# Kernel optimization log

Hardware: AMD Instinct MI355X
Metric: run time of the kernel (lower is better)

## Reference

```python
import jax, jax.numpy as jnp
import numpy as np

B, L, D, H = 2, 384, 256, 8
DH = D // H


def setup_inputs() -> dict:
    key = jax.random.key(0)
    ks = jax.random.split(key, 16)
    xav = lambda k, shape: jax.random.normal(k, shape, jnp.float32) * np.sqrt(2.0 / sum(shape[-2:]))
    return {
        "key": jax.random.normal(ks[0], (B, L, D), jnp.float32),
        "query": jax.random.normal(ks[1], (B, L, D), jnp.float32),
        "value": jax.random.normal(ks[2], (B, L, D), jnp.float32),
        "pos": jax.random.normal(ks[3], (B, L, L, D), jnp.float32),
        "key_mask": jnp.ones((B, L), jnp.float32),
        "Wk": xav(ks[4], (D, D)), "bk": jnp.zeros((D,), jnp.float32),
        "Wq": xav(ks[5], (D, D)), "bq": jnp.zeros((D,), jnp.float32),
        "Wv": xav(ks[6], (D, D)), "bv": jnp.zeros((D,), jnp.float32),
        "Wr": xav(ks[7], (D, D)), "br": jnp.zeros((D,), jnp.float32),
        "u": xav(ks[8], (H, DH)),
        "v": xav(ks[9], (H, DH)),
    }


def reference(key, query, value, pos, key_mask, Wk, bk, Wq, bq, Wv, bv, Wr, br, u, v):
    b, l, d = key.shape
    dh = d // H
    # projections (torch Linear: x @ W.T + b)
    k = (key @ Wk.T + bk).reshape(b, l, H, dh).transpose(0, 2, 1, 3)    # [b,h,l,dh]
    q = (query @ Wq.T + bq).reshape(b, l, H, dh).transpose(0, 2, 1, 3)  # [b,h,l,dh]
    val = (value @ Wv.T + bv).reshape(b, l, H, dh).transpose(0, 2, 1, 3)
    r = (pos @ Wr.T + br).reshape(b, l, l, H, dh)                       # [b,q,k,h,dh]
    # content term A+C: (q + u) @ k^T
    A_C = jnp.einsum("bhqd,bhkd->bhqk", q + u[None, :, None, :], k)
    # position term B+D: (q + v) contracted with per-(q,k) relative embedding
    B_D = jnp.einsum("bhqd,bqkhd->bhqk", q + v[None, :, None, :], r)
    score = (A_C + B_D) / np.sqrt(dh).astype(np.float32)
    score = score - (1.0 - key_mask[:, None, None, :]) * 1e15
    attn = jax.nn.softmax(score, axis=-1)  # dropout is identity at eval
    out = jnp.einsum("bhqk,bhkd->bhqd", attn, val)
    return out.transpose(0, 2, 1, 3).reshape(b, l, d)
```

## Files before the change

### kernel.cpp

```cpp
#include <hip/hip_runtime.h>
#include <math.h>

#define BB 2
#define LL 384
#define DD 256
#define HH 8
#define DHH 32

static const size_t OFF_Q     = 0;
static const size_t OFF_KK    = 196608;
static const size_t OFF_VV    = 393216;
static const size_t OFF_W     = 589824;
static const size_t OFF_CBR   = 2162688;
static const size_t OFF_SCORE = 2168832;

__device__ __forceinline__ float dot4(float4 a, float4 b) {
    return a.x * b.x + a.y * b.y + a.z * b.z + a.w * b.w;
}

__global__ __launch_bounds__(256) void k_proj(
    const float* __restrict__ Xq, const float* __restrict__ Xk, const float* __restrict__ Xv,
    const float* __restrict__ Wq, const float* __restrict__ Wk, const float* __restrict__ Wv,
    const float* __restrict__ bq, const float* __restrict__ bk, const float* __restrict__ bv,
    float* __restrict__ oq, float* __restrict__ okk, float* __restrict__ ovv)
{
    int bx = blockIdx.x;
    int mat = bx / 96;
    int rem = bx % 96;
    int b = rem / 48;
    int l0 = (rem % 48) * 8;
    const float* X = (mat == 0) ? Xq : (mat == 1) ? Xk : Xv;
    const float* W = (mat == 0) ? Wq : (mat == 1) ? Wk : Wv;
    const float* bias = (mat == 0) ? bq : (mat == 1) ? bk : bv;

    __shared__ float xs[8 * 256];
    int tid = threadIdx.x;
    {
        const float4* src = (const float4*)(X + (size_t)(b * LL + l0) * DD);
        float4* dst = (float4*)xs;
        dst[tid] = src[tid];
        dst[tid + 256] = src[tid + 256];
    }
    __syncthreads();

    int n = tid;
    float bn = bias[n];
    float acc[8];
#pragma unroll
    for (int l = 0; l < 8; ++l) acc[l] = bn;

    const float4* wrow = (const float4*)(W + (size_t)n * DD);
#pragma unroll 8
    for (int kc = 0; kc < 64; ++kc) {
        float4 wv = wrow[kc];
#pragma unroll
        for (int l = 0; l < 8; ++l) {
            float4 xv = ((const float4*)(xs + l * 256))[kc];
            acc[l] += dot4(wv, xv);
        }
    }

    if (mat == 0) {
#pragma unroll
        for (int l = 0; l < 8; ++l)
            oq[(size_t)(b * LL + l0 + l) * DD + n] = acc[l];
    } else {
        float* o = (mat == 1) ? okk : ovv;
        int h = n >> 5, dh = n & 31;
#pragma unroll
        for (int l = 0; l < 8; ++l)
            o[((size_t)(b * HH + h) * LL + l0 + l) * DHH + dh] = acc[l];
    }
}

__global__ __launch_bounds__(256) void k_wproj(
    const float* __restrict__ q, const float* __restrict__ vpar,
    const float* __restrict__ Wr, const float* __restrict__ br,
    float* __restrict__ w, float* __restrict__ cbr)
{
    int b = blockIdx.x / 96;
    int l0 = (blockIdx.x % 96) * 4;
    int tid = threadIdx.x;
    int gq = tid >> 6;
    int lane = tid & 63;

    __shared__ float qv[4][256];
    {
        const float4* qsrc = (const float4*)(q + (size_t)(b * LL + l0 + gq) * DD);
        const float4* vsrc = (const float4*)vpar;
        float4 t = qsrc[lane];
        float4 vv4 = vsrc[lane];
        t.x += vv4.x; t.y += vv4.y; t.z += vv4.z; t.w += vv4.w;
        ((float4*)qv[gq])[lane] = t;
    }
    __syncthreads();

    int l = l0 + gq;
    int d4 = lane * 4;
    float* wbase = w + ((size_t)(b * LL + l) * HH) * DD + d4;
    for (int h = 0; h < HH; ++h) {
        float4 acc = make_float4(0.f, 0.f, 0.f, 0.f);
#pragma unroll 8
        for (int dh = 0; dh < 32; ++dh) {
            float s = qv[gq][h * 32 + dh];
            float4 wr4 = *(const float4*)(Wr + (size_t)(h * 32 + dh) * DD + d4);
            acc.x += s * wr4.x; acc.y += s * wr4.y; acc.z += s * wr4.z; acc.w += s * wr4.w;
        }
        *(float4*)(wbase + h * DD) = acc;
    }

    if (tid < 32) {
        int g2 = tid >> 3, hh = tid & 7;
        float s = 0.f;
#pragma unroll 8
        for (int dh = 0; dh < 32; ++dh)
            s += qv[g2][hh * 32 + dh] * br[hh * 32 + dh];
        cbr[(size_t)(b * LL + l0 + g2) * HH + hh] = s;
    }
}

__global__ __launch_bounds__(256) void k_bd(
    const float* __restrict__ pos, const float* __restrict__ w,
    float* __restrict__ score)
{
    int b = blockIdx.x / LL;
    int qi = blockIdx.x % LL;
    int tid = threadIdx.x;
    int wave = tid >> 6;
    int lane = tid & 63;
    int g = lane & 15;
    int r = lane >> 4;

    const float* wb = w + ((size_t)(b * LL + qi) * HH) * DD + g * 4;
    float4 wr[8][4];
#pragma unroll
    for (int h = 0; h < 8; ++h) {
#pragma unroll
        for (int j = 0; j < 4; ++j)
            wr[h][j] = *(const float4*)(wb + h * DD + j * 64);
    }

    const float* posq = pos + (size_t)(b * LL + qi) * LL * DD + g * 4;
    float* sb = score + ((size_t)(b * HH) * LL + qi) * LL;
    const float inv = 0.17677669529663687f;

#pragma unroll 1
    for (int k0 = wave * 4; k0 < LL; k0 += 16) {
        int krow = k0 + r;
        const float* pr = posq + (size_t)krow * DD;
        float4 p0 = *(const float4*)(pr);
        float4 p1 = *(const float4*)(pr + 64);
        float4 p2 = *(const float4*)(pr + 128);
        float4 p3 = *(const float4*)(pr + 192);
        float acc[8];
#pragma unroll
        for (int h = 0; h < 8; ++h)
            acc[h] = dot4(p0, wr[h][0]) + dot4(p1, wr[h][1]) +
                     dot4(p2, wr[h][2]) + dot4(p3, wr[h][3]);
#pragma unroll
        for (int m = 1; m <= 8; m <<= 1) {
#pragma unroll
            for (int h = 0; h < 8; ++h)
                acc[h] += __shfl_xor(acc[h], m, 64);
        }
        if (g == 0) {
#pragma unroll
            for (int h = 0; h < 8; ++h)
                sb[(size_t)h * LL * LL + krow] = acc[h] * inv;
        }
    }
}

__global__ __launch_bounds__(384) void k_ac(
    const float* __restrict__ q, const float* __restrict__ u,
    const float* __restrict__ kk, const float* __restrict__ cbr,
    const float* __restrict__ mask, float* __restrict__ score)
{
    int bx = blockIdx.x;
    int qt = bx & 15;
    int bh = bx >> 4;
    int b = bh >> 3;
    int h = bh & 7;
    int q0 = qt * 24;
    int tid = threadIdx.x;

    __shared__ float qu[24][32];
    __shared__ float cb[24];
    for (int idx = tid; idx < 768; idx += 384) {
        int ql = idx >> 5, dh = idx & 31;
        qu[ql][dh] = q[(size_t)(b * LL + q0 + ql) * DD + h * 32 + dh] + u[h * 32 + dh];
    }
    if (tid < 24) cb[tid] = cbr[(size_t)(b * LL + q0 + tid) * HH + h];

    float4 kr[8];
    const float4* kbase = (const float4*)(kk + ((size_t)(b * HH + h) * LL + tid) * DHH);
#pragma unroll
    for (int j = 0; j < 8; ++j) kr[j] = kbase[j];
    float pen = (1.0f - mask[b * LL + tid]) * 1e15f;
    __syncthreads();

    const float inv = 0.17677669529663687f;
    float* srow = score + ((size_t)(b * HH + h) * LL + q0) * LL + tid;
    for (int ql = 0; ql < 24; ++ql) {
        const float4* qp = (const float4*)qu[ql];
        float acc = 0.f;
#pragma unroll
        for (int j = 0; j < 8; ++j) acc += dot4(qp[j], kr[j]);
        float* sp = srow + (size_t)ql * LL;
        *sp = *sp + (acc + cb[ql]) * inv - pen;
    }
}

__global__ __launch_bounds__(256) void k_softpv(
    const float* __restrict__ score, const float* __restrict__ vv,
    float* __restrict__ out)
{
    int bx = blockIdx.x;
    int qt = bx % 48;
    int bh = bx / 48;
    int b = bh >> 3;
    int h = bh & 7;
    int q0 = qt * 8;
    int tid = threadIdx.x;

    __shared__ float valT[32][388];
    __shared__ float attn[8][388];

    const float* vb = vv + (size_t)(b * HH + h) * LL * DHH;
    for (int i = 0; i < 48; ++i) {
        int flat = i * 256 + tid;
        valT[flat & 31][flat >> 5] = vb[flat];
    }

    int wave = tid >> 6, lane = tid & 63;
    for (int ri = 0; ri < 2; ++ri) {
        int ql = wave * 2 + ri;
        const float* srow = score + ((size_t)(b * HH + h) * LL + q0 + ql) * LL;
        float s[6];
#pragma unroll
        for (int j = 0; j < 6; ++j) s[j] = srow[lane + 64 * j];
        float m = s[0];
#pragma unroll
        for (int j = 1; j < 6; ++j) m = fmaxf(m, s[j]);
#pragma unroll
        for (int off = 1; off < 64; off <<= 1) m = fmaxf(m, __shfl_xor(m, off, 64));
        float e[6];
        float ls = 0.f;
#pragma unroll
        for (int j = 0; j < 6; ++j) { e[j] = __expf(s[j] - m); ls += e[j]; }
#pragma unroll
        for (int off = 1; off < 64; off <<= 1) ls += __shfl_xor(ls, off, 64);
        float rinv = 1.0f / ls;
#pragma unroll
        for (int j = 0; j < 6; ++j) attn[ql][lane + 64 * j] = e[j] * rinv;
    }
    __syncthreads();

    int dh = tid & 31, qp = tid >> 5;
    const float4* vrow = (const float4*)valT[dh];
    const float4* arow = (const float4*)attn[qp];
    float acc = 0.f;
    for (int k4 = 0; k4 < 96; ++k4) {
        acc += dot4(arow[k4], vrow[k4]);
    }
    out[(size_t)(b * LL + q0 + qp) * DD + h * 32 + dh] = acc;
}

extern "C" void kernel_launch(void* const* d_in, const int* in_sizes, int n_in,
                              void* d_out, int out_size, void* d_ws, size_t ws_size,
                              hipStream_t stream) {
    const float* key    = (const float*)d_in[0];
    const float* query  = (const float*)d_in[1];
    const float* value  = (const float*)d_in[2];
    const float* pos    = (const float*)d_in[3];
    const float* kmask  = (const float*)d_in[4];
    const float* Wk     = (const float*)d_in[5];
    const float* bk     = (const float*)d_in[6];
    const float* Wq     = (const float*)d_in[7];
    const float* bq     = (const float*)d_in[8];
    const float* Wv     = (const float*)d_in[9];
    const float* bv     = (const float*)d_in[10];
    const float* Wr     = (const float*)d_in[11];
    const float* br     = (const float*)d_in[12];
    const float* u      = (const float*)d_in[13];
    const float* v      = (const float*)d_in[14];
    float* out = (float*)d_out;

    float* ws = (float*)d_ws;
    float* qbuf   = ws + OFF_Q;
    float* kkbuf  = ws + OFF_KK;
    float* vvbuf  = ws + OFF_VV;
    float* wbuf   = ws + OFF_W;
    float* cbrbuf = ws + OFF_CBR;
    float* sbuf   = ws + OFF_SCORE;

    k_proj<<<dim3(288), dim3(256), 0, stream>>>(query, key, value, Wq, Wk, Wv,
                                                bq, bk, bv, qbuf, kkbuf, vvbuf);
    k_wproj<<<dim3(192), dim3(256), 0, stream>>>(qbuf, v, Wr, br, wbuf, cbrbuf);
    k_bd<<<dim3(768), dim3(256), 0, stream>>>(pos, wbuf, sbuf);
    k_ac<<<dim3(256), dim3(384), 0, stream>>>(qbuf, u, kkbuf, cbrbuf, kmask, sbuf);
    k_softpv<<<dim3(768), dim3(256), 0, stream>>>(sbuf, vvbuf, out);
}
```

Measured before the change: 500.6 us.

## Fuse content score term into position-score kernel and split Wr projection by head groups

The content term (q+u)·k, the bias term and the key mask are now computed inside the position-score kernel, so the separate k_ac kernel and its read-modify-write pass over the score buffer go away. K is now stored in row-major [b,l,D] layout so each 16-lane group can read contiguous float2 slices per head next to the pos rows. The Wr projection kernel is split across four head groups, raising its grid from 192 to 768 blocks for more parallelism. k_bd gets a launch bound asking for 2 blocks per SM, which may cap registers and cause spills given the large wr array it holds.

```diff
diff --git a/kernel.cpp b/kernel.cpp
--- a/kernel.cpp
+++ b/kernel.cpp
@@ -60,16 +60,16 @@
         }
     }
 
-    if (mat == 0) {
+    if (mat <= 1) {
+        float* o = (mat == 0) ? oq : okk;
 #pragma unroll
         for (int l = 0; l < 8; ++l)
-            oq[(size_t)(b * LL + l0 + l) * DD + n] = acc[l];
+            o[(size_t)(b * LL + l0 + l) * DD + n] = acc[l];
     } else {
-        float* o = (mat == 1) ? okk : ovv;
         int h = n >> 5, dh = n & 31;
 #pragma unroll
         for (int l = 0; l < 8; ++l)
-            o[((size_t)(b * HH + h) * LL + l0 + l) * DHH + dh] = acc[l];
+            ovv[((size_t)(b * HH + h) * LL + l0 + l) * DHH + dh] = acc[l];
     }
 }
 
@@ -78,50 +78,57 @@
     const float* __restrict__ Wr, const float* __restrict__ br,
     float* __restrict__ w, float* __restrict__ cbr)
 {
-    int b = blockIdx.x / 96;
-    int l0 = (blockIdx.x % 96) * 4;
+    int bx = blockIdx.x;
+    int b = bx / 384;
+    int rem = bx % 384;
+    int l0 = (rem >> 2) * 4;
+    int hg = rem & 3;
     int tid = threadIdx.x;
     int gq = tid >> 6;
     int lane = tid & 63;
 
-    __shared__ float qv[4][256];
-    {
-        const float4* qsrc = (const float4*)(q + (size_t)(b * LL + l0 + gq) * DD);
-        const float4* vsrc = (const float4*)vpar;
-        float4 t = qsrc[lane];
-        float4 vv4 = vsrc[lane];
+    __shared__ float qv[4][64];
+    if (lane < 16) {
+        const float* qsrc = q + (size_t)(b * LL + l0 + gq) * DD + hg * 64;
+        const float* vsrc = vpar + hg * 64;
+        float4 t = *(const float4*)(qsrc + lane * 4);
+        float4 vv4 = *(const float4*)(vsrc + lane * 4);
         t.x += vv4.x; t.y += vv4.y; t.z += vv4.z; t.w += vv4.w;
-        ((float4*)qv[gq])[lane] = t;
+        *(float4*)(&qv[gq][lane * 4]) = t;
     }
     __syncthreads();
 
     int l = l0 + gq;
     int d4 = lane * 4;
     float* wbase = w + ((size_t)(b * LL + l) * HH) * DD + d4;
-    for (int h = 0; h < HH; ++h) {
+#pragma unroll
+    for (int h2 = 0; h2 < 2; ++h2) {
+        int h = hg * 2 + h2;
         float4 acc = make_float4(0.f, 0.f, 0.f, 0.f);
 #pragma unroll 8
         for (int dh = 0; dh < 32; ++dh) {
-            float s = qv[gq][h * 32 + dh];
+            float s = qv[gq][h2 * 32 + dh];
             float4 wr4 = *(const float4*)(Wr + (size_t)(h * 32 + dh) * DD + d4);
             acc.x += s * wr4.x; acc.y += s * wr4.y; acc.z += s * wr4.z; acc.w += s * wr4.w;
         }
         *(float4*)(wbase + h * DD) = acc;
     }
 
-    if (tid < 32) {
-        int g2 = tid >> 3, hh = tid & 7;
+    if (tid < 8) {
+        int rr = tid >> 1, h2 = tid & 1;
         float s = 0.f;
 #pragma unroll 8
         for (int dh = 0; dh < 32; ++dh)
-            s += qv[g2][hh * 32 + dh] * br[hh * 32 + dh];
-        cbr[(size_t)(b * LL + l0 + g2) * HH + hh] = s;
-    }
-}
-
-__global__ __launch_bounds__(256) void k_bd(
+            s += qv[rr][h2 * 32 + dh] * br[hg * 64 + h2 * 32 + dh];
+        cbr[(size_t)(b * LL + l0 + rr) * HH + hg * 2 + h2] = s;
+    }
+}
+
+__global__ __launch_bounds__(256, 2) void k_bd(
     const float* __restrict__ pos, const float* __restrict__ w,
-    float* __restrict__ score)
+    const float* __restrict__ q, const float* __restrict__ u,
+    const float* __restrict__ kk, const float* __restrict__ cbr,
+    const float* __restrict__ mask, float* __restrict__ score)
 {
     int b = blockIdx.x / LL;
     int qi = blockIdx.x % LL;
@@ -140,7 +147,20 @@
             wr[h][j] = *(const float4*)(wb + h * DD + j * 64);
     }
 
+    float2 qu[8];
+    const float* qrow = q + (size_t)(b * LL + qi) * DD + 2 * g;
+#pragma unroll
+    for (int h = 0; h < 8; ++h) {
+        float2 qa = *(const float2*)(qrow + h * 32);
+        float2 ua = *(const float2*)(u + h * 32 + 2 * g);
+        qu[h] = make_float2(qa.x + ua.x, qa.y + ua.y);
+    }
+    float cb[8];
+#pragma unroll
+    for (int h = 0; h < 8; ++h) cb[h] = cbr[(size_t)(b * LL + qi) * HH + h];
+
     const float* posq = pos + (size_t)(b * LL + qi) * LL * DD + g * 4;
+    const float* kkb = kk + (size_t)b * LL * DD + 2 * g;
     float* sb = score + ((size_t)(b * HH) * LL + qi) * LL;
     const float inv = 0.17677669529663687f;
 
@@ -152,11 +172,15 @@
         float4 p1 = *(const float4*)(pr + 64);
         float4 p2 = *(const float4*)(pr + 128);
         float4 p3 = *(const float4*)(pr + 192);
+        const float* kr = kkb + (size_t)krow * DD;
         float acc[8];
 #pragma unroll
-        for (int h = 0; h < 8; ++h)
+        for (int h = 0; h < 8; ++h) {
+            float2 kv = *(const float2*)(kr + h * 32);
             acc[h] = dot4(p0, wr[h][0]) + dot4(p1, wr[h][1]) +
-                     dot4(p2, wr[h][2]) + dot4(p3, wr[h][3]);
+                     dot4(p2, wr[h][2]) + dot4(p3, wr[h][3]) +
+                     qu[h].x * kv.x + qu[h].y * kv.y;
+        }
 #pragma unroll
         for (int m = 1; m <= 8; m <<= 1) {
 #pragma unroll
@@ -164,50 +188,11 @@
                 acc[h] += __shfl_xor(acc[h], m, 64);
         }
         if (g == 0) {
+            float pen = (1.0f - mask[b * LL + krow]) * 1e15f;
 #pragma unroll
             for (int h = 0; h < 8; ++h)
-                sb[(size_t)h * LL * LL + krow] = acc[h] * inv;
-        }
-    }
-}
-
-__global__ __launch_bounds__(384) void k_ac(
-    const float* __restrict__ q, const float* __restrict__ u,
-    const float* __restrict__ kk, const float* __restrict__ cbr,
-    const float* __restrict__ mask, float* __restrict__ score)
-{
-    int bx = blockIdx.x;
-    int qt = bx & 15;
-    int bh = bx >> 4;
-    int b = bh >> 3;
-    int h = bh & 7;
-    int q0 = qt * 24;
-    int tid = threadIdx.x;
-
-    __shared__ float qu[24][32];
-    __shared__ float cb[24];
-    for (int idx = tid; idx < 768; idx += 384) {
-        int ql = idx >> 5, dh = idx & 31;
-        qu[ql][dh] = q[(size_t)(b * LL + q0 + ql) * DD + h * 32 + dh] + u[h * 32 + dh];
-    }
-    if (tid < 24) cb[tid] = cbr[(size_t)(b * LL + q0 + tid) * HH + h];
-
-    float4 kr[8];
-    const float4* kbase = (const float4*)(kk + ((size_t)(b * HH + h) * LL + tid) * DHH);
-#pragma unroll
-    for (int j = 0; j < 8; ++j) kr[j] = kbase[j];
-    float pen = (1.0f - mask[b * LL + tid]) * 1e15f;
-    __syncthreads();
-
-    const float inv = 0.17677669529663687f;
-    float* srow = score + ((size_t)(b * HH + h) * LL + q0) * LL + tid;
-    for (int ql = 0; ql < 24; ++ql) {
-        const float4* qp = (const float4*)qu[ql];
-        float acc = 0.f;
-#pragma unroll
-        for (int j = 0; j < 8; ++j) acc += dot4(qp[j], kr[j]);
-        float* sp = srow + (size_t)ql * LL;
-        *sp = *sp + (acc + cb[ql]) * inv - pen;
+                sb[(size_t)h * LL * LL + krow] = (acc[h] + cb[h]) * inv - pen;
+        }
     }
 }
 
@@ -296,8 +281,8 @@
 
     k_proj<<<dim3(288), dim3(256), 0, stream>>>(query, key, value, Wq, Wk, Wv,
                                                 bq, bk, bv, qbuf, kkbuf, vvbuf);
-    k_wproj<<<dim3(192), dim3(256), 0, stream>>>(qbuf, v, Wr, br, wbuf, cbrbuf);
-    k_bd<<<dim3(768), dim3(256), 0, stream>>>(pos, wbuf, sbuf);
-    k_ac<<<dim3(256), dim3(384), 0, stream>>>(qbuf, u, kkbuf, cbrbuf, kmask, sbuf);
+    k_wproj<<<dim3(768), dim3(256), 0, stream>>>(qbuf, v, Wr, br, wbuf, cbrbuf);
+    k_bd<<<dim3(768), dim3(256), 0, stream>>>(pos, wbuf, qbuf, u, kkbuf, cbrbuf,
+                                              kmask, sbuf);
     k_softpv<<<dim3(768), dim3(256), 0, stream>>>(sbuf, vvbuf, out);
 }
```

Result: no change. 506.4 us (+1.2%).
